# Performance work log

Measured on AMD Instinct MI355X. Metric: run time of the kernel, lower is better.

The kernel has to match this reference:

```python
import math
import jax, jax.numpy as jnp
import numpy as np

B, S, D_MODEL = 4, 2048, 512
H, D_KV = 8, 64
NUM_BUCKETS = 32
MAX_DISTANCE = 128  # T5 default


def _relative_position_bucket(rel_pos, bidirectional=True, num_buckets=NUM_BUCKETS, max_distance=MAX_DISTANCE):
    # Standard T5 bucketing (encoder: bidirectional=True since is_decoder=False).
    ret = jnp.zeros_like(rel_pos)
    if bidirectional:
        num_buckets //= 2
        ret = (rel_pos > 0).astype(jnp.int32) * num_buckets
        rel_pos = jnp.abs(rel_pos)
    else:
        rel_pos = -jnp.minimum(rel_pos, 0)
    max_exact = num_buckets // 2
    is_small = rel_pos < max_exact
    safe_rp = jnp.maximum(rel_pos, 1)  # avoid log(0); masked out by is_small
    val_if_large = max_exact + (
        jnp.log(safe_rp.astype(jnp.float32) / max_exact)
        / math.log(max_distance / max_exact)
        * (num_buckets - max_exact)
    ).astype(jnp.int32)
    val_if_large = jnp.minimum(val_if_large, num_buckets - 1)
    return ret + jnp.where(is_small, rel_pos, val_if_large)


def setup_inputs() -> dict:
    key = jax.random.key(0)
    ks = jax.random.split(key, 8)
    query = jax.random.normal(ks[0], (B, S, D_MODEL), dtype=jnp.float32)
    kk = jax.random.normal(ks[1], (B, S, D_MODEL), dtype=jnp.float32)
    vv = jax.random.normal(ks[2], (B, S, D_MODEL), dtype=jnp.float32)
    key_mask = jnp.ones((B, S), dtype=jnp.float32)
    scale = 1.0 / math.sqrt(D_MODEL)
    Wq = jax.random.normal(ks[3], (D_MODEL, H * D_KV), dtype=jnp.float32) * scale
    Wk = jax.random.normal(ks[4], (D_MODEL, H * D_KV), dtype=jnp.float32) * scale
    Wv = jax.random.normal(ks[5], (D_MODEL, H * D_KV), dtype=jnp.float32) * scale
    rel_emb = jax.random.normal(ks[6], (NUM_BUCKETS, H), dtype=jnp.float32) * 0.1
    return {"query": query, "key": kk, "value": vv, "key_mask": key_mask,
            "Wq": Wq, "Wk": Wk, "Wv": Wv, "rel_emb": rel_emb, "start_pos": 0}


def reference(query, key, value, key_mask, Wq, Wk, Wv, rel_emb, start_pos):
    Bq, Q, _ = query.shape
    K = key.shape[1]
    # projections (training path: no cache; equals start_pos=0 prefill)
    q = (query @ Wq).reshape(Bq, Q, H, D_KV)  # [B,Q,H,d]
    k = (key @ Wk).reshape(Bq, K, H, D_KV)
    v = (value @ Wv).reshape(Bq, K, H, D_KV)
    # T5: no 1/sqrt(d) scaling
    scores = jnp.einsum("bqhd,bkhd->bhqk", q, k)  # [B,H,Q,K]
    # relative position bias over [K,K], sliced to last Q rows
    ctx = jnp.arange(K)[:, None]
    mem = jnp.arange(K)[None, :]
    buckets = _relative_position_bucket(mem - ctx)  # [K,K]
    bias = rel_emb[buckets]  # [K,K,H]
    bias = jnp.transpose(bias, (2, 0, 1))[None, :, -Q:, :]  # [1,H,Q,K]
    scores = scores + bias
    # additive key mask
    add_mask = (1.0 - key_mask)[:, None, None, :] * -10000.0
    scores = scores + add_mask
    probs = jax.nn.softmax(scores, axis=-1)
    context = jnp.einsum("bhqk,bkhd->bqhd", probs, v)
    return context.reshape(Bq, Q, H * D_KV)
```

## Files before the change

### kernel.cpp

```cpp
#include <hip/hip_runtime.h>
#include <hip/hip_bf16.h>

typedef __attribute__((ext_vector_type(8))) _Float16 half8;
typedef __attribute__((ext_vector_type(4))) float f32x4;

#define LOG2E 1.4426950408889634f

__global__ __launch_bounds__(256) void cvt_h_kernel(const float* __restrict__ q,
                                                    const float* __restrict__ k,
                                                    const float* __restrict__ v,
                                                    _Float16* __restrict__ xq,
                                                    _Float16* __restrict__ xk,
                                                    _Float16* __restrict__ xv) {
  const int z = blockIdx.y;
  const float* x = z == 0 ? q : z == 1 ? k : v;
  _Float16* y = z == 0 ? xq : z == 1 ? xk : xv;
  size_t i = (size_t)blockIdx.x * 256 + threadIdx.x;
  const f32x4* p = (const f32x4*)x + i * 2;
  f32x4 a = p[0], b = p[1];
  half8 o;
  o[0] = (_Float16)a[0]; o[1] = (_Float16)a[1];
  o[2] = (_Float16)a[2]; o[3] = (_Float16)a[3];
  o[4] = (_Float16)b[0]; o[5] = (_Float16)b[1];
  o[6] = (_Float16)b[2]; o[7] = (_Float16)b[3];
  ((half8*)y)[i] = o;
}

__global__ __launch_bounds__(256) void wtrans_kernel(const float* __restrict__ Wq,
                                                     const float* __restrict__ Wk,
                                                     const float* __restrict__ Wv,
                                                     _Float16* __restrict__ wtq,
                                                     _Float16* __restrict__ wtk,
                                                     _Float16* __restrict__ wtv) {
  const int z = blockIdx.z;
  const float* W = z == 0 ? Wq : z == 1 ? Wk : Wv;
  _Float16* Wt = z == 0 ? wtq : z == 1 ? wtk : wtv;
  __shared__ float tile[32][33];
  int k0 = blockIdx.x * 32, n0 = blockIdx.y * 32;
  int c = threadIdx.x & 31, r0 = threadIdx.x >> 5;
  #pragma unroll
  for (int rr = 0; rr < 32; rr += 8)
    tile[r0 + rr][c] = W[(size_t)(k0 + r0 + rr) * 512 + n0 + c];
  __syncthreads();
  #pragma unroll
  for (int rr = 0; rr < 32; rr += 8)
    Wt[(size_t)(n0 + r0 + rr) * 512 + k0 + c] = (_Float16)tile[c][r0 + rr];
}

__global__ __launch_bounds__(256) void proj_kernel(const _Float16* __restrict__ Xq,
                                                   const _Float16* __restrict__ Xk,
                                                   const _Float16* __restrict__ Xv,
                                                   const _Float16* __restrict__ Wtq,
                                                   const _Float16* __restrict__ Wtk,
                                                   const _Float16* __restrict__ Wtv,
                                                   _Float16* __restrict__ Qp,
                                                   _Float16* __restrict__ Kp,
                                                   _Float16* __restrict__ Vt) {
  const int z = blockIdx.z;
  const _Float16* X  = z == 0 ? Xq : z == 1 ? Xk : Xv;
  const _Float16* Wt = z == 0 ? Wtq : z == 1 ? Wtk : Wtv;
  _Float16* outp     = z == 0 ? Qp : z == 1 ? Kp : Vt;

  __shared__ __align__(16) char lt_all[4 * 64 * 144];
  const int wave = threadIdx.x >> 6, lane = threadIdx.x & 63;
  const int g = lane >> 4, li = lane & 15;
  const int m0 = blockIdx.x * 128 + wave * 32;
  const int h = blockIdx.y;

  f32x4 acc[2][4];
  #pragma unroll
  for (int i = 0; i < 2; ++i)
    #pragma unroll
    for (int j = 0; j < 4; ++j) acc[i][j] = (f32x4){0.f, 0.f, 0.f, 0.f};

  const _Float16* xa = X + (size_t)m0 * 512;
  const _Float16* wb = Wt + (size_t)(h << 6) * 512;

  for (int k0 = 0; k0 < 512; k0 += 32) {
    half8 a[2], bw[4];
    #pragma unroll
    for (int rt = 0; rt < 2; ++rt)
      a[rt] = *(const half8*)(xa + (size_t)(rt * 16 + li) * 512 + k0 + g * 8);
    #pragma unroll
    for (int ct = 0; ct < 4; ++ct)
      bw[ct] = *(const half8*)(wb + (size_t)(ct * 16 + li) * 512 + k0 + g * 8);
    #pragma unroll
    for (int rt = 0; rt < 2; ++rt)
      #pragma unroll
      for (int ct = 0; ct < 4; ++ct)
        acc[rt][ct] = __builtin_amdgcn_mfma_f32_16x16x32_f16(a[rt], bw[ct], acc[rt][ct], 0, 0, 0);
  }

  const int bidx = m0 >> 11, sbase = m0 & 2047;
  if (z != 2) {
    #pragma unroll
    for (int rt = 0; rt < 2; ++rt)
      #pragma unroll
      for (int r = 0; r < 4; ++r) {
        int s = sbase + rt * 16 + g * 4 + r;
        _Float16* orow = outp + ((size_t)((bidx * 8 + h) * 2048 + s) << 6);
        #pragma unroll
        for (int ct = 0; ct < 4; ++ct)
          orow[ct * 16 + li] = (_Float16)acc[rt][ct][r];
      }
  } else {
    char* lt = lt_all + wave * (64 * 144);
    #pragma unroll
    for (int rt = 0; rt < 2; ++rt)
      #pragma unroll
      for (int ct = 0; ct < 4; ++ct)
        #pragma unroll
        for (int r = 0; r < 4; ++r) {
          int d = ct * 16 + li, sl = rt * 16 + g * 4 + r;
          *(_Float16*)(lt + d * 144 + ((sl * 2) ^ ((d & 7) << 4))) = (_Float16)acc[rt][ct][r];
        }
    __syncthreads();
    int d = lane;
    _Float16* vrow = outp + (size_t)((bidx * 8 + h) * 64 + d) * 2048 + sbase;
    #pragma unroll
    for (int c = 0; c < 4; ++c) {
      half8 vv = *(half8*)(lt + d * 144 + ((c * 16) ^ ((d & 7) << 4)));
      *(half8*)(vrow + c * 8) = vv;
    }
  }
}

__global__ __launch_bounds__(128) void attn_kernel(const _Float16* __restrict__ Qp,
                                                   const _Float16* __restrict__ Kp,
                                                   const _Float16* __restrict__ Vt,
                                                   const float* __restrict__ kmask,
                                                   const float* __restrict__ rel_emb,
                                                   float* __restrict__ outp) {
  __shared__ float bias_tab[4096];
  __shared__ __align__(16) char pb_all[2 * 4096];
  const int bh = blockIdx.y, b = bh >> 3, h = bh & 7;
  const int wave = threadIdx.x >> 6, lane = threadIdx.x & 63;
  const int g = lane >> 4, li = lane & 15;
  const int qw = blockIdx.x * 64 + wave * 32;

  for (int idx = (int)threadIdx.x; idx < 4095; idx += 128) {
    int rel = idx - 2047;
    int ret = rel > 0 ? 16 : 0;
    int rp = rel < 0 ? -rel : rel;
    int bb;
    if (rp < 8) bb = rp;
    else {
      int t = (rp >= 12) + (rp >= 16) + (rp >= 23) + (rp >= 32) +
              (rp >= 46) + (rp >= 64) + (rp >= 91);
      bb = 8 + t;
    }
    bias_tab[idx] = rel_emb[(ret + bb) * 8 + h];
  }
  const float bias_far_neg = rel_emb[15 * 8 + h];
  const float bias_far_pos = rel_emb[31 * 8 + h];

  const _Float16* Qb = Qp + (size_t)bh * (2048 * 64);
  const _Float16* Kb = Kp + (size_t)bh * (2048 * 64);
  const _Float16* Vb = Vt + (size_t)bh * (64 * 2048);
  const float* mkb = kmask + b * 2048;

  half8 qa[2][2];
  #pragma unroll
  for (int rt = 0; rt < 2; ++rt)
    #pragma unroll
    for (int kc = 0; kc < 2; ++kc)
      qa[rt][kc] = *(const half8*)(Qb + (size_t)(qw + rt * 16 + li) * 64 + kc * 32 + g * 8);

  f32x4 o[2][4];
  float mrow[2][4], lrow[2][4];
  #pragma unroll
  for (int rt = 0; rt < 2; ++rt) {
    #pragma unroll
    for (int ct = 0; ct < 4; ++ct) o[rt][ct] = (f32x4){0.f, 0.f, 0.f, 0.f};
    #pragma unroll
    for (int r = 0; r < 4; ++r) { mrow[rt][r] = -1e30f; lrow[rt][r] = 0.f; }
  }
  char* pb = pb_all + wave * 4096;

  __syncthreads();

  for (int j0 = 0; j0 < 2048; j0 += 64) {
    half8 kb[4][2];
    #pragma unroll
    for (int jt = 0; jt < 4; ++jt)
      #pragma unroll
      for (int kc = 0; kc < 2; ++kc)
        kb[jt][kc] = *(const half8*)(Kb + (size_t)(j0 + jt * 16 + li) * 64 + kc * 32 + g * 8);
    float mterm[4];
    #pragma unroll
    for (int jt = 0; jt < 4; ++jt)
      mterm[jt] = (1.0f - mkb[j0 + jt * 16 + li]) * -10000.0f;

    f32x4 sc[2][4];
    __builtin_amdgcn_s_setprio(1);
    #pragma unroll
    for (int rt = 0; rt < 2; ++rt)
      #pragma unroll
      for (int jt = 0; jt < 4; ++jt) {
        f32x4 z = (f32x4){0.f, 0.f, 0.f, 0.f};
        z = __builtin_amdgcn_mfma_f32_16x16x32_f16(qa[rt][0], kb[jt][0], z, 0, 0, 0);
        sc[rt][jt] = __builtin_amdgcn_mfma_f32_16x16x32_f16(qa[rt][1], kb[jt][1], z, 0, 0, 0);
      }
    __builtin_amdgcn_s_setprio(0);

    #pragma unroll
    for (int rt = 0; rt < 2; ++rt)
      #pragma unroll
      for (int jt = 0; jt < 4; ++jt) {
        int jlo = j0 + jt * 16, qlo = qw + rt * 16;
        if (jlo - (qlo + 15) >= 91) {
          #pragma unroll
          for (int r = 0; r < 4; ++r) sc[rt][jt][r] += bias_far_pos + mterm[jt];
        } else if ((jlo + 15) - qlo <= -91) {
          #pragma unroll
          for (int r = 0; r < 4; ++r) sc[rt][jt][r] += bias_far_neg + mterm[jt];
        } else {
          #pragma unroll
          for (int r = 0; r < 4; ++r)
            sc[rt][jt][r] += bias_tab[(jlo + li) - (qlo + g * 4 + r) + 2047] + mterm[jt];
        }
      }

    float lmax[2][4];
    int need = 0;
    #pragma unroll
    for (int rt = 0; rt < 2; ++rt)
      #pragma unroll
      for (int r = 0; r < 4; ++r) {
        lmax[rt][r] = fmaxf(fmaxf(sc[rt][0][r], sc[rt][1][r]),
                            fmaxf(sc[rt][2][r], sc[rt][3][r]));
        need |= (lmax[rt][r] - mrow[rt][r] > 8.0f);
      }
    if (__any(need)) {
      #pragma unroll
      for (int rt = 0; rt < 2; ++rt) {
        #pragma unroll
        for (int r = 0; r < 4; ++r) {
          float t = lmax[rt][r];
          t = fmaxf(t, __shfl_xor(t, 1));
          t = fmaxf(t, __shfl_xor(t, 2));
          t = fmaxf(t, __shfl_xor(t, 4));
          t = fmaxf(t, __shfl_xor(t, 8));
          float mnew = fmaxf(mrow[rt][r], t);
          float scal = exp2f((mrow[rt][r] - mnew) * LOG2E);
          mrow[rt][r] = mnew;
          lrow[rt][r] *= scal;
          #pragma unroll
          for (int ct = 0; ct < 4; ++ct) o[rt][ct][r] *= scal;
        }
      }
    }
    #pragma unroll
    for (int rt = 0; rt < 2; ++rt)
      #pragma unroll
      for (int r = 0; r < 4; ++r) {
        float ps = 0.f;
        #pragma unroll
        for (int jt = 0; jt < 4; ++jt) {
          float p = exp2f((sc[rt][jt][r] - mrow[rt][r]) * LOG2E);
          sc[rt][jt][r] = p;
          ps += p;
        }
        lrow[rt][r] += ps;
      }

    #pragma unroll
    for (int rt = 0; rt < 2; ++rt)
      #pragma unroll
      for (int jt = 0; jt < 4; ++jt)
        #pragma unroll
        for (int r = 0; r < 4; ++r) {
          int row = rt * 16 + g * 4 + r, col = jt * 16 + li;
          *(_Float16*)(pb + row * 128 + ((col * 2) ^ ((row & 7) << 4))) =
              (_Float16)sc[rt][jt][r];
        }
    half8 pa[2][2];
    #pragma unroll
    for (int rt = 0; rt < 2; ++rt)
      #pragma unroll
      for (int jc = 0; jc < 2; ++jc) {
        int row = rt * 16 + li;
        pa[rt][jc] = *(half8*)(pb + row * 128 + (((jc * 32 + g * 8) * 2) ^ ((row & 7) << 4)));
      }

    __builtin_amdgcn_s_setprio(1);
    #pragma unroll
    for (int dct = 0; dct < 4; ++dct) {
      half8 vb0 = *(const half8*)(Vb + (size_t)(dct * 16 + li) * 2048 + j0 + g * 8);
      half8 vb1 = *(const half8*)(Vb + (size_t)(dct * 16 + li) * 2048 + j0 + 32 + g * 8);
      #pragma unroll
      for (int rt = 0; rt < 2; ++rt) {
        o[rt][dct] = __builtin_amdgcn_mfma_f32_16x16x32_f16(pa[rt][0], vb0, o[rt][dct], 0, 0, 0);
        o[rt][dct] = __builtin_amdgcn_mfma_f32_16x16x32_f16(pa[rt][1], vb1, o[rt][dct], 0, 0, 0);
      }
    }
    __builtin_amdgcn_s_setprio(0);
  }

  #pragma unroll
  for (int rt = 0; rt < 2; ++rt)
    #pragma unroll
    for (int r = 0; r < 4; ++r) {
      float t = lrow[rt][r];
      t += __shfl_xor(t, 1);
      t += __shfl_xor(t, 2);
      t += __shfl_xor(t, 4);
      t += __shfl_xor(t, 8);
      float inv = 1.0f / t;
      int qrow = qw + rt * 16 + g * 4 + r;
      float* orow = outp + ((size_t)b * 2048 + qrow) * 512 + h * 64;
      #pragma unroll
      for (int ct = 0; ct < 4; ++ct)
        orow[ct * 16 + li] = o[rt][ct][r] * inv;
    }
}

extern "C" void kernel_launch(void* const* d_in, const int* in_sizes, int n_in,
                              void* d_out, int out_size, void* d_ws, size_t ws_size,
                              hipStream_t stream) {
  const float* query = (const float*)d_in[0];
  const float* key   = (const float*)d_in[1];
  const float* value = (const float*)d_in[2];
  const float* kmask = (const float*)d_in[3];
  const float* Wq    = (const float*)d_in[4];
  const float* Wk    = (const float*)d_in[5];
  const float* Wv    = (const float*)d_in[6];
  const float* rel   = (const float*)d_in[7];

  char* ws = (char*)d_ws;
  const size_t SZB = 8192ull * 512 * 2;
  const size_t WB  = 512ull * 512 * 2;
  _Float16* xq  = (_Float16*)(ws);
  _Float16* xk  = (_Float16*)(ws + SZB);
  _Float16* xv  = (_Float16*)(ws + 2 * SZB);
  _Float16* wtq = (_Float16*)(ws + 3 * SZB);
  _Float16* wtk = (_Float16*)(ws + 3 * SZB + WB);
  _Float16* wtv = (_Float16*)(ws + 3 * SZB + 2 * WB);
  _Float16* qp  = (_Float16*)(ws + 3 * SZB + 3 * WB);
  _Float16* kp  = (_Float16*)(ws + 4 * SZB + 3 * WB);
  _Float16* vt  = (_Float16*)(ws + 5 * SZB + 3 * WB);

  cvt_h_kernel<<<dim3(2048, 3), dim3(256), 0, stream>>>(query, key, value, xq, xk, xv);
  wtrans_kernel<<<dim3(16, 16, 3), dim3(256), 0, stream>>>(Wq, Wk, Wv, wtq, wtk, wtv);
  proj_kernel<<<dim3(64, 8, 3), dim3(256), 0, stream>>>(xq, xk, xv, wtq, wtk, wtv, qp, kp, vt);
  attn_kernel<<<dim3(32, 32), dim3(128), 0, stream>>>(qp, kp, vt, kmask, rel, (float*)d_out);
}
```

Measured before the change: 310.0 us.

## Restructure attention to single-wave 16-row blocks with transposed S=K·Qᵀ MFMA

Rewrites the attention kernel so each 64-thread block handles 16 query rows, and computes scores as K·Qᵀ so each lane owns a single query row. Row max and sum then need only two cross-lane shuffles, and the lazy-rescale threshold is dropped in favour of an unconditional rescale. LOG2E is folded into the Q projection and the bias table, the bias table shrinks to 256 entries, the mask is loaded as vectors, and P is packed to fp16 with cvt_pkrtz. Output stores become float4 writes. The grid grows fourfold, which gives more blocks and occupancy, but K and V are re-read by four times as many blocks.

```diff
diff --git a/kernel.cpp b/kernel.cpp
--- a/kernel.cpp
+++ b/kernel.cpp
@@ -2,6 +2,7 @@
 #include <hip/hip_bf16.h>
 
 typedef __attribute__((ext_vector_type(8))) _Float16 half8;
+typedef __attribute__((ext_vector_type(2))) __fp16 fp16x2;
 typedef __attribute__((ext_vector_type(4))) float f32x4;
 
 #define LOG2E 1.4426950408889634f
@@ -91,6 +92,7 @@
         acc[rt][ct] = __builtin_amdgcn_mfma_f32_16x16x32_f16(a[rt], bw[ct], acc[rt][ct], 0, 0, 0);
   }
 
+  const float qs = (z == 0) ? LOG2E : 1.0f;
   const int bidx = m0 >> 11, sbase = m0 & 2047;
   if (z != 2) {
     #pragma unroll
@@ -101,7 +103,7 @@
         _Float16* orow = outp + ((size_t)((bidx * 8 + h) * 2048 + s) << 6);
         #pragma unroll
         for (int ct = 0; ct < 4; ++ct)
-          orow[ct * 16 + li] = (_Float16)acc[rt][ct][r];
+          orow[ct * 16 + li] = (_Float16)(acc[rt][ct][r] * qs);
       }
   } else {
     char* lt = lt_all + wave * (64 * 144);
@@ -125,21 +127,21 @@
   }
 }
 
-__global__ __launch_bounds__(128) void attn_kernel(const _Float16* __restrict__ Qp,
-                                                   const _Float16* __restrict__ Kp,
-                                                   const _Float16* __restrict__ Vt,
-                                                   const float* __restrict__ kmask,
-                                                   const float* __restrict__ rel_emb,
-                                                   float* __restrict__ outp) {
-  __shared__ float bias_tab[4096];
-  __shared__ __align__(16) char pb_all[2 * 4096];
+__global__ __launch_bounds__(64, 4) void attn_kernel(const _Float16* __restrict__ Qp,
+                                                     const _Float16* __restrict__ Kp,
+                                                     const _Float16* __restrict__ Vt,
+                                                     const float* __restrict__ kmask,
+                                                     const float* __restrict__ rel_emb,
+                                                     float* __restrict__ outp) {
+  __shared__ float bias_tab[256];
+  __shared__ __align__(16) char pb[2048];
   const int bh = blockIdx.y, b = bh >> 3, h = bh & 7;
-  const int wave = threadIdx.x >> 6, lane = threadIdx.x & 63;
+  const int lane = threadIdx.x;
   const int g = lane >> 4, li = lane & 15;
-  const int qw = blockIdx.x * 64 + wave * 32;
-
-  for (int idx = (int)threadIdx.x; idx < 4095; idx += 128) {
-    int rel = idx - 2047;
+  const int qw = blockIdx.x * 16;
+
+  for (int idx = lane; idx < 256; idx += 64) {
+    int rel = idx - 128;
     int ret = rel > 0 ? 16 : 0;
     int rp = rel < 0 ? -rel : rel;
     int bb;
@@ -149,34 +151,28 @@
               (rp >= 46) + (rp >= 64) + (rp >= 91);
       bb = 8 + t;
     }
-    bias_tab[idx] = rel_emb[(ret + bb) * 8 + h];
-  }
-  const float bias_far_neg = rel_emb[15 * 8 + h];
-  const float bias_far_pos = rel_emb[31 * 8 + h];
+    bias_tab[idx] = rel_emb[(ret + bb) * 8 + h] * LOG2E;
+  }
+  const float far_neg = rel_emb[15 * 8 + h] * LOG2E;
+  const float far_pos = rel_emb[31 * 8 + h] * LOG2E;
+  const float MASKC = 10000.0f * LOG2E;
 
   const _Float16* Qb = Qp + (size_t)bh * (2048 * 64);
   const _Float16* Kb = Kp + (size_t)bh * (2048 * 64);
   const _Float16* Vb = Vt + (size_t)bh * (64 * 2048);
   const float* mkb = kmask + b * 2048;
 
-  half8 qa[2][2];
-  #pragma unroll
-  for (int rt = 0; rt < 2; ++rt)
-    #pragma unroll
-    for (int kc = 0; kc < 2; ++kc)
-      qa[rt][kc] = *(const half8*)(Qb + (size_t)(qw + rt * 16 + li) * 64 + kc * 32 + g * 8);
-
-  f32x4 o[2][4];
-  float mrow[2][4], lrow[2][4];
-  #pragma unroll
-  for (int rt = 0; rt < 2; ++rt) {
-    #pragma unroll
-    for (int ct = 0; ct < 4; ++ct) o[rt][ct] = (f32x4){0.f, 0.f, 0.f, 0.f};
-    #pragma unroll
-    for (int r = 0; r < 4; ++r) { mrow[rt][r] = -1e30f; lrow[rt][r] = 0.f; }
-  }
-  char* pb = pb_all + wave * 4096;
-
+  half8 qa[2];
+  #pragma unroll
+  for (int kc = 0; kc < 2; ++kc)
+    qa[kc] = *(const half8*)(Qb + (size_t)(qw + li) * 64 + kc * 32 + g * 8);
+
+  f32x4 o[4];
+  #pragma unroll
+  for (int ct = 0; ct < 4; ++ct) o[ct] = (f32x4){0.f, 0.f, 0.f, 0.f};
+  float m = -1e30f, l = 0.f;
+
+  const int swz = (li & 7) << 4;
   __syncthreads();
 
   for (int j0 = 0; j0 < 2048; j0 += 64) {
@@ -186,133 +182,86 @@
       #pragma unroll
       for (int kc = 0; kc < 2; ++kc)
         kb[jt][kc] = *(const half8*)(Kb + (size_t)(j0 + jt * 16 + li) * 64 + kc * 32 + g * 8);
-    float mterm[4];
+
+    f32x4 sc[4];
+    #pragma unroll
+    for (int jt = 0; jt < 4; ++jt) {
+      f32x4 zz = (f32x4){0.f, 0.f, 0.f, 0.f};
+      zz = __builtin_amdgcn_mfma_f32_16x16x32_f16(kb[jt][0], qa[0], zz, 0, 0, 0);
+      sc[jt] = __builtin_amdgcn_mfma_f32_16x16x32_f16(kb[jt][1], qa[1], zz, 0, 0, 0);
+    }
+
+    #pragma unroll
+    for (int jt = 0; jt < 4; ++jt) {
+      int jlo = j0 + jt * 16;
+      f32x4 m4 = *(const f32x4*)(mkb + jlo + 4 * g);
+      if (jlo - (qw + 15) >= 91) {
+        #pragma unroll
+        for (int r = 0; r < 4; ++r)
+          sc[jt][r] += far_pos + (m4[r] - 1.0f) * MASKC;
+      } else if (jlo + 15 - qw <= -91) {
+        #pragma unroll
+        for (int r = 0; r < 4; ++r)
+          sc[jt][r] += far_neg + (m4[r] - 1.0f) * MASKC;
+      } else {
+        int base = jlo + 4 * g - qw - li + 128;
+        #pragma unroll
+        for (int r = 0; r < 4; ++r)
+          sc[jt][r] += bias_tab[base + r] + (m4[r] - 1.0f) * MASKC;
+      }
+    }
+
+    float t = sc[0][0];
     #pragma unroll
     for (int jt = 0; jt < 4; ++jt)
-      mterm[jt] = (1.0f - mkb[j0 + jt * 16 + li]) * -10000.0f;
-
-    f32x4 sc[2][4];
-    __builtin_amdgcn_s_setprio(1);
-    #pragma unroll
-    for (int rt = 0; rt < 2; ++rt)
-      #pragma unroll
-      for (int jt = 0; jt < 4; ++jt) {
-        f32x4 z = (f32x4){0.f, 0.f, 0.f, 0.f};
-        z = __builtin_amdgcn_mfma_f32_16x16x32_f16(qa[rt][0], kb[jt][0], z, 0, 0, 0);
-        sc[rt][jt] = __builtin_amdgcn_mfma_f32_16x16x32_f16(qa[rt][1], kb[jt][1], z, 0, 0, 0);
-      }
-    __builtin_amdgcn_s_setprio(0);
-
-    #pragma unroll
-    for (int rt = 0; rt < 2; ++rt)
-      #pragma unroll
-      for (int jt = 0; jt < 4; ++jt) {
-        int jlo = j0 + jt * 16, qlo = qw + rt * 16;
-        if (jlo - (qlo + 15) >= 91) {
-          #pragma unroll
-          for (int r = 0; r < 4; ++r) sc[rt][jt][r] += bias_far_pos + mterm[jt];
-        } else if ((jlo + 15) - qlo <= -91) {
-          #pragma unroll
-          for (int r = 0; r < 4; ++r) sc[rt][jt][r] += bias_far_neg + mterm[jt];
-        } else {
-          #pragma unroll
-          for (int r = 0; r < 4; ++r)
-            sc[rt][jt][r] += bias_tab[(jlo + li) - (qlo + g * 4 + r) + 2047] + mterm[jt];
-        }
-      }
-
-    float lmax[2][4];
-    int need = 0;
-    #pragma unroll
-    for (int rt = 0; rt < 2; ++rt)
-      #pragma unroll
-      for (int r = 0; r < 4; ++r) {
-        lmax[rt][r] = fmaxf(fmaxf(sc[rt][0][r], sc[rt][1][r]),
-                            fmaxf(sc[rt][2][r], sc[rt][3][r]));
-        need |= (lmax[rt][r] - mrow[rt][r] > 8.0f);
-      }
-    if (__any(need)) {
-      #pragma unroll
-      for (int rt = 0; rt < 2; ++rt) {
-        #pragma unroll
-        for (int r = 0; r < 4; ++r) {
-          float t = lmax[rt][r];
-          t = fmaxf(t, __shfl_xor(t, 1));
-          t = fmaxf(t, __shfl_xor(t, 2));
-          t = fmaxf(t, __shfl_xor(t, 4));
-          t = fmaxf(t, __shfl_xor(t, 8));
-          float mnew = fmaxf(mrow[rt][r], t);
-          float scal = exp2f((mrow[rt][r] - mnew) * LOG2E);
-          mrow[rt][r] = mnew;
-          lrow[rt][r] *= scal;
-          #pragma unroll
-          for (int ct = 0; ct < 4; ++ct) o[rt][ct][r] *= scal;
-        }
-      }
-    }
-    #pragma unroll
-    for (int rt = 0; rt < 2; ++rt)
-      #pragma unroll
-      for (int r = 0; r < 4; ++r) {
-        float ps = 0.f;
-        #pragma unroll
-        for (int jt = 0; jt < 4; ++jt) {
-          float p = exp2f((sc[rt][jt][r] - mrow[rt][r]) * LOG2E);
-          sc[rt][jt][r] = p;
-          ps += p;
-        }
-        lrow[rt][r] += ps;
-      }
-
-    #pragma unroll
-    for (int rt = 0; rt < 2; ++rt)
-      #pragma unroll
-      for (int jt = 0; jt < 4; ++jt)
-        #pragma unroll
-        for (int r = 0; r < 4; ++r) {
-          int row = rt * 16 + g * 4 + r, col = jt * 16 + li;
-          *(_Float16*)(pb + row * 128 + ((col * 2) ^ ((row & 7) << 4))) =
-              (_Float16)sc[rt][jt][r];
-        }
-    half8 pa[2][2];
-    #pragma unroll
-    for (int rt = 0; rt < 2; ++rt)
-      #pragma unroll
-      for (int jc = 0; jc < 2; ++jc) {
-        int row = rt * 16 + li;
-        pa[rt][jc] = *(half8*)(pb + row * 128 + (((jc * 32 + g * 8) * 2) ^ ((row & 7) << 4)));
-      }
-
+      #pragma unroll
+      for (int r = 0; r < 4; ++r) t = fmaxf(t, sc[jt][r]);
+    t = fmaxf(t, __shfl_xor(t, 16));
+    t = fmaxf(t, __shfl_xor(t, 32));
+    float mnew = fmaxf(m, t);
+    float scal = exp2f(m - mnew);
+    m = mnew;
+    l *= scal;
+    #pragma unroll
+    for (int ct = 0; ct < 4; ++ct) o[ct] *= scal;
+
+    #pragma unroll
+    for (int jt = 0; jt < 4; ++jt) {
+      float p0 = exp2f(sc[jt][0] - m), p1 = exp2f(sc[jt][1] - m);
+      float p2 = exp2f(sc[jt][2] - m), p3 = exp2f(sc[jt][3] - m);
+      l += (p0 + p1) + (p2 + p3);
+      fp16x2 h01 = __builtin_amdgcn_cvt_pkrtz(p0, p1);
+      fp16x2 h23 = __builtin_amdgcn_cvt_pkrtz(p2, p3);
+      uint2 w;
+      w.x = __builtin_bit_cast(unsigned, h01);
+      w.y = __builtin_bit_cast(unsigned, h23);
+      *(uint2*)(pb + li * 128 + ((32 * jt + 8 * g) ^ swz)) = w;
+    }
+
+    half8 pa0 = *(half8*)(pb + li * 128 + ((16 * g) ^ swz));
+    half8 pa1 = *(half8*)(pb + li * 128 + ((64 + 16 * g) ^ swz));
     __builtin_amdgcn_s_setprio(1);
     #pragma unroll
     for (int dct = 0; dct < 4; ++dct) {
       half8 vb0 = *(const half8*)(Vb + (size_t)(dct * 16 + li) * 2048 + j0 + g * 8);
       half8 vb1 = *(const half8*)(Vb + (size_t)(dct * 16 + li) * 2048 + j0 + 32 + g * 8);
-      #pragma unroll
-      for (int rt = 0; rt < 2; ++rt) {
-        o[rt][dct] = __builtin_amdgcn_mfma_f32_16x16x32_f16(pa[rt][0], vb0, o[rt][dct], 0, 0, 0);
-        o[rt][dct] = __builtin_amdgcn_mfma_f32_16x16x32_f16(pa[rt][1], vb1, o[rt][dct], 0, 0, 0);
-      }
+      o[dct] = __builtin_amdgcn_mfma_f32_16x16x32_f16(vb0, pa0, o[dct], 0, 0, 0);
+      o[dct] = __builtin_amdgcn_mfma_f32_16x16x32_f16(vb1, pa1, o[dct], 0, 0, 0);
     }
     __builtin_amdgcn_s_setprio(0);
   }
 
-  #pragma unroll
-  for (int rt = 0; rt < 2; ++rt)
-    #pragma unroll
-    for (int r = 0; r < 4; ++r) {
-      float t = lrow[rt][r];
-      t += __shfl_xor(t, 1);
-      t += __shfl_xor(t, 2);
-      t += __shfl_xor(t, 4);
-      t += __shfl_xor(t, 8);
-      float inv = 1.0f / t;
-      int qrow = qw + rt * 16 + g * 4 + r;
-      float* orow = outp + ((size_t)b * 2048 + qrow) * 512 + h * 64;
-      #pragma unroll
-      for (int ct = 0; ct < 4; ++ct)
-        orow[ct * 16 + li] = o[rt][ct][r] * inv;
-    }
+  float lf = l;
+  lf += __shfl_xor(lf, 16);
+  lf += __shfl_xor(lf, 32);
+  float inv = 1.0f / lf;
+  float* orow = outp + ((size_t)b * 2048 + qw + li) * 512 + h * 64;
+  #pragma unroll
+  for (int dct = 0; dct < 4; ++dct) {
+    f32x4 ov = o[dct];
+    ov[0] *= inv; ov[1] *= inv; ov[2] *= inv; ov[3] *= inv;
+    *(f32x4*)(orow + dct * 16 + 4 * g) = ov;
+  }
 }
 
 extern "C" void kernel_launch(void* const* d_in, const int* in_sizes, int n_in,
@@ -343,5 +292,5 @@
   cvt_h_kernel<<<dim3(2048, 3), dim3(256), 0, stream>>>(query, key, value, xq, xk, xv);
   wtrans_kernel<<<dim3(16, 16, 3), dim3(256), 0, stream>>>(Wq, Wk, Wv, wtq, wtk, wtv);
   proj_kernel<<<dim3(64, 8, 3), dim3(256), 0, stream>>>(xq, xk, xv, wtq, wtk, wtv, qp, kp, vt);
-  attn_kernel<<<dim3(32, 32), dim3(128), 0, stream>>>(qp, kp, vt, kmask, rel, (float*)d_out);
-}
+  attn_kernel<<<dim3(128, 32), dim3(64), 0, stream>>>(qp, kp, vt, kmask, rel, (float*)d_out);
+}
```

Result: slower. 431.7 us (+39.3%).
